# Performance work log

Hardware: AMD Instinct MI355X
Metric: run time of the kernel (lower is better)

The kernel has to match this reference:

```python
import jax, jax.numpy as jnp
import numpy as np

N_NODES = 50000
N_EDGES = 800000
DROP_P = 0.1


def setup_inputs() -> dict:
    key = jax.random.key(0)
    ks = jax.random.split(key, 8)
    x = jax.random.normal(ks[0], (N_NODES, 128), dtype=jnp.float32)
    edge_index = jax.random.randint(ks[1], (2, N_EDGES), 0, N_NODES, dtype=jnp.int64)
    # SAGEConv params: lin_l (applied to aggregated neighbors, has bias), lin_r (root, no bias)
    Wl1 = jax.random.normal(ks[2], (128, 256), dtype=jnp.float32) * 0.05
    Wr1 = jax.random.normal(ks[3], (128, 256), dtype=jnp.float32) * 0.05
    b1 = jax.random.normal(ks[4], (256,), dtype=jnp.float32) * 0.05
    Wl2 = jax.random.normal(ks[5], (256, 128), dtype=jnp.float32) * 0.05
    Wr2 = jax.random.normal(ks[6], (256, 128), dtype=jnp.float32) * 0.05
    b2 = jax.random.normal(ks[7], (128,), dtype=jnp.float32) * 0.05
    return {"x": x, "edge_index": edge_index, "Wl1": Wl1, "Wr1": Wr1, "b1": b1,
            "Wl2": Wl2, "Wr2": Wr2, "b2": b2}


def _sage_conv(x, src, dst, Wl, Wr, b, n_nodes):
    # PyG SAGEConv (mean aggr): out = lin_l(mean_{j in N(i)} x_j) + lin_r(x_i)
    msg = x[src]                                                  # [E, d] gather
    agg = jax.ops.segment_sum(msg, dst, num_segments=n_nodes)    # [N, d]
    cnt = jax.ops.segment_sum(jnp.ones((src.shape[0],), x.dtype), dst, num_segments=n_nodes)
    mean = agg / jnp.maximum(cnt, 1.0)[:, None]
    return mean @ Wl + x @ Wr + b


def reference(x, edge_index, Wl1, Wr1, b1, Wl2, Wr2, b2):
    src, dst = edge_index[0], edge_index[1]
    n = x.shape[0]
    h = _sage_conv(x, src, dst, Wl1, Wr1, b1, n)
    h = jax.nn.relu(h)
    # dropout p=0.1 with deterministic key (training=True in source)
    keep = jax.random.bernoulli(jax.random.key(42), 1.0 - DROP_P, h.shape)
    h = jnp.where(keep, h / (1.0 - DROP_P), 0.0)
    return _sage_conv(h, src, dst, Wl2, Wr2, b2, n)
```

## Files before the change

kernel.cpp:

```cpp
#include <hip/hip_runtime.h>

#define NN 50000
#define NE 800000
#define NBC 49
#define MSB 782

typedef __attribute__((ext_vector_type(8))) short short8;
typedef __attribute__((ext_vector_type(4))) float f32x4;

#define GLDS(g, l)                                                              \
  __builtin_amdgcn_global_load_lds(                                             \
      (const __attribute__((address_space(1))) void*)(g),                       \
      (__attribute__((address_space(3))) void*)(l), 16, 0, 0)

__device__ __forceinline__ unsigned short f2bf(float f) {
  union { float f; unsigned u; } v; v.f = f;
  unsigned r = (v.u + 0x7FFFu + ((v.u >> 16) & 1u)) >> 16;
  return (unsigned short)r;
}
__device__ __forceinline__ float bflo(unsigned u) {
  union { unsigned x; float f; } v; v.x = u << 16; return v.f;
}
__device__ __forceinline__ float bfhi(unsigned u) {
  union { unsigned x; float f; } v; v.x = u & 0xFFFF0000u; return v.f;
}

__device__ __forceinline__ unsigned tf_rotl(unsigned x, int r) {
#if __has_builtin(__builtin_amdgcn_alignbit)
  return __builtin_amdgcn_alignbit(x, x, 32 - r);
#else
  return (x << r) | (x >> (32 - r));
#endif
}
__device__ __forceinline__ void threefry_0_42(unsigned x0, unsigned x1,
                                              unsigned& o0, unsigned& o1) {
  const unsigned k0 = 0u, k1 = 42u;
  const unsigned k2 = k0 ^ k1 ^ 0x1BD11BDAu;
  x0 += k0; x1 += k1;
#define TF_R(r) { x0 += x1; x1 = tf_rotl(x1, (r)); x1 ^= x0; }
  TF_R(13) TF_R(15) TF_R(26) TF_R(6)
  x0 += k1; x1 += k2 + 1u;
  TF_R(17) TF_R(29) TF_R(16) TF_R(24)
  x0 += k2; x1 += k0 + 2u;
  TF_R(13) TF_R(15) TF_R(26) TF_R(6)
  x0 += k0; x1 += k1 + 3u;
  TF_R(17) TF_R(29) TF_R(16) TF_R(24)
  x0 += k1; x1 += k2 + 4u;
  TF_R(13) TF_R(15) TF_R(26) TF_R(6)
  x0 += k2; x1 += k0 + 5u;
#undef TF_R
  o0 = x0; o1 = x1;
}

#define CVTB 6250
#define MSKW 400000
#define MSKB 1563
__global__ void prep_k(const float4* __restrict__ x, uint2* __restrict__ xb,
                       const float* __restrict__ Wl1, const float* __restrict__ Wr1,
                       const float* __restrict__ Wl2, const float* __restrict__ Wr2,
                       unsigned short* __restrict__ W1t, unsigned short* __restrict__ W2t,
                       unsigned* __restrict__ msk, unsigned* __restrict__ hist) {
  int bid = blockIdx.x;
  if (bid < CVTB) {
    int i = bid * 256 + threadIdx.x;
    float4 v = x[i];
    uint2 o;
    o.x = (unsigned)f2bf(v.x) | ((unsigned)f2bf(v.y) << 16);
    o.y = (unsigned)f2bf(v.z) | ((unsigned)f2bf(v.w) << 16);
    xb[i] = o;
  } else if (bid < CVTB + 512) {
    int gid = (bid - CVTB) * 256 + threadIdx.x;
    int idx = gid & 65535;
    int n = idx >> 8, k = idx & 255;
    if (gid < 65536) {
      float v = (k < 128) ? Wr1[(size_t)k * 256 + n] : Wl1[(size_t)(k - 128) * 256 + n];
      W1t[idx] = f2bf(v);
    } else {
      float v = (n < 128) ? Wl2[(size_t)k * 128 + n] : Wr2[(size_t)k * 128 + (n - 128)];
      W2t[idx] = f2bf(v);
    }
  } else if (bid < CVTB + 512 + MSKB) {
    int w = (bid - CVTB - 512) * 256 + threadIdx.x;
    if (w < MSKW) {
      unsigned base = (unsigned)w * 32u;
      unsigned m = 0;
#pragma unroll
      for (int b = 0; b < 32; ++b) {
        unsigned o0, o1;
        threefry_0_42(0u, base + (unsigned)b, o0, o1);
        if (((o0 ^ o1) >> 9) < 7549747u) m |= (1u << b);
      }
      msk[w] = m;
    }
  } else {
    if (threadIdx.x < 64) hist[threadIdx.x] = 0;
  }
}

__global__ __launch_bounds__(256) void histC_k(const int* __restrict__ dst,
                                               unsigned* __restrict__ hist) {
  __shared__ unsigned lh[64];
  int tid = threadIdx.x;
  if (tid < 64) lh[tid] = 0;
  __syncthreads();
  int base = blockIdx.x * 1024;
#pragma unroll
  for (int k = 0; k < 4; ++k) {
    int e = base + k * 256 + tid;
    if (e < NE) atomicAdd(&lh[((unsigned)dst[e]) >> 10], 1u);
  }
  __syncthreads();
  if (tid < 64 && lh[tid]) atomicAdd(&hist[tid], lh[tid]);
}

__global__ __launch_bounds__(64) void scan64_k(const unsigned* __restrict__ hist,
                                               unsigned* __restrict__ bases,
                                               unsigned* __restrict__ gcur) {
  int tid = threadIdx.x;
  unsigned v = hist[tid], incl = v;
#pragma unroll
  for (int o = 1; o < 64; o <<= 1) {
    unsigned t = __shfl_up(incl, o);
    if (tid >= o) incl += t;
  }
  unsigned ex = incl - v;
  bases[tid] = ex;
  gcur[tid] = ex;
  if (tid == 63) bases[64] = incl;
}

__global__ __launch_bounds__(256) void msplit_k(const int* __restrict__ src,
                                                const int* __restrict__ dst,
                                                unsigned* __restrict__ gcur,
                                                unsigned* __restrict__ bufA) {
  __shared__ unsigned lh[64], gb[64], lc[64];
  int tid = threadIdx.x;
  if (tid < 64) { lh[tid] = 0; lc[tid] = 0; }
  __syncthreads();
  int base = blockIdx.x * 1024;
  unsigned s[4], d[4];
  bool val[4];
#pragma unroll
  for (int k = 0; k < 4; ++k) {
    int e = base + k * 256 + tid;
    val[k] = (e < NE);
    s[k] = val[k] ? (unsigned)src[e] : 0u;
    d[k] = val[k] ? (unsigned)dst[e] : 0u;
    if (val[k]) atomicAdd(&lh[d[k] >> 10], 1u);
  }
  __syncthreads();
  if (tid < 64 && lh[tid]) gb[tid] = atomicAdd(&gcur[tid], lh[tid]);
  __syncthreads();
#pragma unroll
  for (int k = 0; k < 4; ++k) {
    if (val[k]) {
      unsigned b = d[k] >> 10;
      unsigned pos = atomicAdd(&lc[b], 1u);
      bufA[gb[b] + pos] = (s[k] & 0xFFFFu) | ((d[k] & 1023u) << 16);
    }
  }
}

__global__ __launch_bounds__(1024) void passB2_k(const unsigned* __restrict__ bases,
                                                 const unsigned* __restrict__ bufA,
                                                 unsigned short* __restrict__ esrc,
                                                 unsigned* __restrict__ rowptr,
                                                 float* __restrict__ inv) {
  __shared__ unsigned cnt[1024], offs[1024], s_[1024];
  __shared__ unsigned short stage[18432];
  const int b = blockIdx.x, tid = threadIdx.x;
  const unsigned base0 = bases[b];
  const unsigned end0 = bases[b + 1];
  const unsigned bcnt = end0 - base0;

  cnt[tid] = 0;
  __syncthreads();
  for (unsigned i = tid; i < bcnt; i += 1024)
    atomicAdd(&cnt[bufA[base0 + i] >> 16], 1u);
  __syncthreads();

  unsigned c = cnt[tid];
  s_[tid] = c;
  __syncthreads();
  for (int o = 1; o < 1024; o <<= 1) {
    unsigned t = (tid >= o) ? s_[tid - o] : 0u;
    __syncthreads();
    s_[tid] += t;
    __syncthreads();
  }
  unsigned ex = s_[tid] - c;
  offs[tid] = ex;
  int node = b * 1024 + tid;
  if (node < NN) {
    rowptr[node] = base0 + ex;
    inv[node] = 1.0f / fmaxf((float)c, 1.0f);
  }
  cnt[tid] = 0;
  if (b == NBC - 1 && tid == 0) rowptr[NN] = NE;
  __syncthreads();

  if (bcnt <= 18432) {
    for (unsigned i = tid; i < bcnt; i += 1024) {
      unsigned w = bufA[base0 + i];
      unsigned dl = w >> 16;
      unsigned pos = atomicAdd(&cnt[dl], 1u);
      stage[offs[dl] + pos] = (unsigned short)w;
    }
    __syncthreads();
    for (unsigned i = tid; i < bcnt; i += 1024) esrc[base0 + i] = stage[i];
  } else {
    for (unsigned i = tid; i < bcnt; i += 1024) {
      unsigned w = bufA[base0 + i];
      unsigned dl = w >> 16;
      unsigned pos = atomicAdd(&cnt[dl], 1u);
      esrc[base0 + offs[dl] + pos] = (unsigned short)w;
    }
  }
}

__global__ __launch_bounds__(256) void gather_mean_k(
    const unsigned short* __restrict__ esrc, const unsigned* __restrict__ rowptr,
    const float* __restrict__ inv, const unsigned* __restrict__ xb,
    unsigned* __restrict__ meanb) {
  int node = blockIdx.x * 4 + (threadIdx.x >> 6);
  if (node >= NN) return;
  int lane = threadIdx.x & 63;
  unsigned beg = rowptr[node], end = rowptr[node + 1];
  float ax = 0.f, ay = 0.f;
  unsigned t = beg;
  for (; t + 8 <= end; t += 8) {
    unsigned v0 = xb[(size_t)esrc[t + 0] * 64 + lane];
    unsigned v1 = xb[(size_t)esrc[t + 1] * 64 + lane];
    unsigned v2 = xb[(size_t)esrc[t + 2] * 64 + lane];
    unsigned v3 = xb[(size_t)esrc[t + 3] * 64 + lane];
    unsigned v4 = xb[(size_t)esrc[t + 4] * 64 + lane];
    unsigned v5 = xb[(size_t)esrc[t + 5] * 64 + lane];
    unsigned v6 = xb[(size_t)esrc[t + 6] * 64 + lane];
    unsigned v7 = xb[(size_t)esrc[t + 7] * 64 + lane];
    ax += ((bflo(v0) + bflo(v1)) + (bflo(v2) + bflo(v3))) +
          ((bflo(v4) + bflo(v5)) + (bflo(v6) + bflo(v7)));
    ay += ((bfhi(v0) + bfhi(v1)) + (bfhi(v2) + bfhi(v3))) +
          ((bfhi(v4) + bfhi(v5)) + (bfhi(v6) + bfhi(v7)));
  }
  for (; t + 4 <= end; t += 4) {
    unsigned v0 = xb[(size_t)esrc[t + 0] * 64 + lane];
    unsigned v1 = xb[(size_t)esrc[t + 1] * 64 + lane];
    unsigned v2 = xb[(size_t)esrc[t + 2] * 64 + lane];
    unsigned v3 = xb[(size_t)esrc[t + 3] * 64 + lane];
    ax += (bflo(v0) + bflo(v1)) + (bflo(v2) + bflo(v3));
    ay += (bfhi(v0) + bfhi(v1)) + (bfhi(v2) + bfhi(v3));
  }
  for (; t < end; ++t) {
    unsigned v0 = xb[(size_t)esrc[t] * 64 + lane];
    ax += bflo(v0); ay += bfhi(v0);
  }
  float sc = inv[node];
  meanb[(size_t)node * 64 + lane] =
      (unsigned)f2bf(ax * sc) | ((unsigned)f2bf(ay * sc) << 16);
}

__global__ __launch_bounds__(256) void gather_add_k(
    const unsigned short* __restrict__ esrc, const unsigned* __restrict__ rowptr,
    const float* __restrict__ inv, const unsigned* __restrict__ P,
    float* __restrict__ out) {
  int node = blockIdx.x * 4 + (threadIdx.x >> 6);
  if (node >= NN) return;
  int lane = threadIdx.x & 63;
  unsigned beg = rowptr[node], end = rowptr[node + 1];
  float ax = 0.f, ay = 0.f;
  unsigned t = beg;
  for (; t + 8 <= end; t += 8) {
    unsigned v0 = P[(size_t)esrc[t + 0] * 64 + lane];
    unsigned v1 = P[(size_t)esrc[t + 1] * 64 + lane];
    unsigned v2 = P[(size_t)esrc[t + 2] * 64 + lane];
    unsigned v3 = P[(size_t)esrc[t + 3] * 64 + lane];
    unsigned v4 = P[(size_t)esrc[t + 4] * 64 + lane];
    unsigned v5 = P[(size_t)esrc[t + 5] * 64 + lane];
    unsigned v6 = P[(size_t)esrc[t + 6] * 64 + lane];
    unsigned v7 = P[(size_t)esrc[t + 7] * 64 + lane];
    ax += ((bflo(v0) + bflo(v1)) + (bflo(v2) + bflo(v3))) +
          ((bflo(v4) + bflo(v5)) + (bflo(v6) + bflo(v7)));
    ay += ((bfhi(v0) + bfhi(v1)) + (bfhi(v2) + bfhi(v3))) +
          ((bfhi(v4) + bfhi(v5)) + (bfhi(v6) + bfhi(v7)));
  }
  for (; t + 4 <= end; t += 4) {
    unsigned v0 = P[(size_t)esrc[t + 0] * 64 + lane];
    unsigned v1 = P[(size_t)esrc[t + 1] * 64 + lane];
    unsigned v2 = P[(size_t)esrc[t + 2] * 64 + lane];
    unsigned v3 = P[(size_t)esrc[t + 3] * 64 + lane];
    ax += (bflo(v0) + bflo(v1)) + (bflo(v2) + bflo(v3));
    ay += (bfhi(v0) + bfhi(v1)) + (bfhi(v2) + bfhi(v3));
  }
  for (; t < end; ++t) {
    unsigned v0 = P[(size_t)esrc[t] * 64 + lane];
    ax += bflo(v0); ay += bfhi(v0);
  }
  float sc = inv[node];
  float2* O = (float2*)out;
  float2 o = O[(size_t)node * 64 + lane];
  o.x += ax * sc;
  o.y += ay * sc;
  O[(size_t)node * 64 + lane] = o;
}


__global__ __launch_bounds__(256) void mgemm1_k(
    const unsigned short* __restrict__ xb, const unsigned short* __restrict__ meanb,
    const unsigned short* __restrict__ W1t, const float* __restrict__ b1,
    const unsigned* __restrict__ msk, unsigned short* __restrict__ h) {
  __shared__ __align__(16) char As[64 * 64 * 2];
  __shared__ __align__(16) char Bs[64 * 64 * 2];
  const int tid = threadIdx.x;
  const int lane = tid & 63, wid = tid >> 6;
  const int wm = (wid >> 1) * 32, wn = (wid & 1) * 32;
  const int r16 = lane & 15, g = lane >> 4;
  const unsigned bid = blockIdx.x;
  const unsigned v_ = (bid & 7u) * 391u + (bid >> 3);
  const int m0 = (int)(v_ >> 2) * 64;
  const int j0 = (int)(v_ & 3u) * 64;
  const int wbase = (tid & ~63);

  const unsigned short* aSrcX[2];
  const unsigned short* aSrcM[2];
  const unsigned short* bSrc[2];
  char* ldsA[2];
  char* ldsB[2];
#pragma unroll
  for (int p = 0; p < 2; ++p) {
    int id = p * 256 + tid;
    int r = id >> 3, cb = id & 7;
    int grow = m0 + r;
    if (grow >= NN) grow = NN - 1;
    int swz = (cb ^ (r & 7)) << 3;
    aSrcX[p] = xb + (size_t)grow * 128 + swz;
    aSrcM[p] = meanb + (size_t)grow * 128 + swz;
    bSrc[p] = W1t + (size_t)(j0 + r) * 256 + swz;
    ldsA[p] = As + ((p * 256 + wbase) << 4);
    ldsB[p] = Bs + ((p * 256 + wbase) << 4);
  }

  int aoff[2][2], boff[2][2];
#pragma unroll
  for (int f = 0; f < 2; ++f)
#pragma unroll
    for (int ks = 0; ks < 2; ++ks) {
      int ar = wm + f * 16 + r16;
      aoff[f][ks] = ar * 128 + ((ks * 64 + g * 16) ^ ((ar & 7) << 4));
      int br = wn + f * 16 + r16;
      boff[f][ks] = br * 128 + ((ks * 64 + g * 16) ^ ((br & 7) << 4));
    }

  f32x4 acc[2][2] = {};

  auto compute = [&]() {
#pragma unroll
    for (int ks = 0; ks < 2; ++ks) {
      short8 af[2], bf[2];
#pragma unroll
      for (int f = 0; f < 2; ++f) {
        af[f] = *(const short8*)(As + aoff[f][ks]);
        bf[f] = *(const short8*)(Bs + boff[f][ks]);
      }
#pragma unroll
      for (int i = 0; i < 2; ++i)
#pragma unroll
        for (int j = 0; j < 2; ++j)
          acc[i][j] = __builtin_amdgcn_mfma_f32_16x16x32_bf16(af[i], bf[j], acc[i][j], 0, 0, 0);
    }
  };

  GLDS(aSrcX[0], ldsA[0]); GLDS(aSrcX[1], ldsA[1]);
  GLDS(bSrc[0], ldsB[0]);  GLDS(bSrc[1], ldsB[1]);
  __syncthreads();
  compute();
  __syncthreads();
  GLDS(aSrcX[0] + 64, ldsA[0]); GLDS(aSrcX[1] + 64, ldsA[1]);
  GLDS(bSrc[0] + 64, ldsB[0]);  GLDS(bSrc[1] + 64, ldsB[1]);
  __syncthreads();
  compute();
  __syncthreads();
  GLDS(aSrcM[0], ldsA[0]);       GLDS(aSrcM[1], ldsA[1]);
  GLDS(bSrc[0] + 128, ldsB[0]);  GLDS(bSrc[1] + 128, ldsB[1]);
  __syncthreads();
  compute();
  __syncthreads();
  GLDS(aSrcM[0] + 64, ldsA[0]);  GLDS(aSrcM[1] + 64, ldsA[1]);
  GLDS(bSrc[0] + 192, ldsB[0]);  GLDS(bSrc[1] + 192, ldsB[1]);
  __syncthreads();
  compute();

#pragma unroll
  for (int i = 0; i < 2; ++i)
#pragma unroll
    for (int j = 0; j < 2; ++j) {
      int col = j0 + wn + j * 16 + r16;
      float bias = b1[col];
#pragma unroll
      for (int q = 0; q < 4; ++q) {
        int row = m0 + wm + i * 16 + g * 4 + q;
        if (row < NN) {
          unsigned flat = (unsigned)row * 256u + (unsigned)col;
          unsigned keep = (msk[flat >> 5] >> (flat & 31u)) & 1u;
          float v = fmaxf(acc[i][j][q] + bias, 0.f) * (keep ? (1.0f / 0.9f) : 0.f);
          h[(size_t)row * 256 + col] = f2bf(v);
        }
      }
    }
}

__global__ __launch_bounds__(256) void mgemm2_k(
    const unsigned short* __restrict__ h, const unsigned short* __restrict__ W2t,
    const float* __restrict__ b2, unsigned short* __restrict__ P,
    float* __restrict__ out) {
  __shared__ __align__(16) char As[64 * 64 * 2];
  __shared__ __align__(16) char Bs[64 * 64 * 2];
  const int tid = threadIdx.x;
  const int lane = tid & 63, wid = tid >> 6;
  const int wm = (wid >> 1) * 32, wn = (wid & 1) * 32;
  const int r16 = lane & 15, g = lane >> 4;
  const unsigned bid = blockIdx.x;
  const unsigned v_ = (bid & 7u) * 391u + (bid >> 3);
  const int m0 = (int)(v_ >> 2) * 64;
  const int j0 = (int)(v_ & 3u) * 64;
  const int wbase = (tid & ~63);

  const unsigned short* aSrc[2];
  const unsigned short* bSrc[2];
  char* ldsA[2];
  char* ldsB[2];
#pragma unroll
  for (int p = 0; p < 2; ++p) {
    int id = p * 256 + tid;
    int r = id >> 3, cb = id & 7;
    int grow = m0 + r;
    if (grow >= NN) grow = NN - 1;
    int swz = (cb ^ (r & 7)) << 3;
    aSrc[p] = h + (size_t)grow * 256 + swz;
    bSrc[p] = W2t + (size_t)(j0 + r) * 256 + swz;
    ldsA[p] = As + ((p * 256 + wbase) << 4);
    ldsB[p] = Bs + ((p * 256 + wbase) << 4);
  }

  int aoff[2][2], boff[2][2];
#pragma unroll
  for (int f = 0; f < 2; ++f)
#pragma unroll
    for (int ks = 0; ks < 2; ++ks) {
      int ar = wm + f * 16 + r16;
      aoff[f][ks] = ar * 128 + ((ks * 64 + g * 16) ^ ((ar & 7) << 4));
      int br = wn + f * 16 + r16;
      boff[f][ks] = br * 128 + ((ks * 64 + g * 16) ^ ((br & 7) << 4));
    }

  f32x4 acc[2][2] = {};

  auto compute = [&]() {
#pragma unroll
    for (int ks = 0; ks < 2; ++ks) {
      short8 af[2], bf[2];
#pragma unroll
      for (int f = 0; f < 2; ++f) {
        af[f] = *(const short8*)(As + aoff[f][ks]);
        bf[f] = *(const short8*)(Bs + boff[f][ks]);
      }
#pragma unroll
      for (int i = 0; i < 2; ++i)
#pragma unroll
        for (int j = 0; j < 2; ++j)
          acc[i][j] = __builtin_amdgcn_mfma_f32_16x16x32_bf16(af[i], bf[j], acc[i][j], 0, 0, 0);
    }
  };

  GLDS(aSrc[0], ldsA[0]); GLDS(aSrc[1], ldsA[1]);
  GLDS(bSrc[0], ldsB[0]); GLDS(bSrc[1], ldsB[1]);
  __syncthreads();
  compute();
  __syncthreads();
  GLDS(aSrc[0] + 64, ldsA[0]); GLDS(aSrc[1] + 64, ldsA[1]);
  GLDS(bSrc[0] + 64, ldsB[0]); GLDS(bSrc[1] + 64, ldsB[1]);
  __syncthreads();
  compute();
  __syncthreads();
  GLDS(aSrc[0] + 128, ldsA[0]); GLDS(aSrc[1] + 128, ldsA[1]);
  GLDS(bSrc[0] + 128, ldsB[0]); GLDS(bSrc[1] + 128, ldsB[1]);
  __syncthreads();
  compute();
  __syncthreads();
  GLDS(aSrc[0] + 192, ldsA[0]); GLDS(aSrc[1] + 192, ldsA[1]);
  GLDS(bSrc[0] + 192, ldsB[0]); GLDS(bSrc[1] + 192, ldsB[1]);
  __syncthreads();
  compute();

#pragma unroll
  for (int i = 0; i < 2; ++i)
#pragma unroll
    for (int j = 0; j < 2; ++j) {
      int col = j0 + wn + j * 16 + r16;
#pragma unroll
      for (int q = 0; q < 4; ++q) {
        int row = m0 + wm + i * 16 + g * 4 + q;
        if (row < NN) {
          if (col < 128) {
            P[(size_t)row * 128 + col] = f2bf(acc[i][j][q]);
          } else {
            out[(size_t)row * 128 + (col - 128)] = acc[i][j][q] + b2[col - 128];
          }
        }
      }
    }
}

extern "C" void kernel_launch(void* const* d_in, const int* in_sizes, int n_in,
                              void* d_out, int out_size, void* d_ws, size_t ws_size,
                              hipStream_t stream) {
  const float* x   = (const float*)d_in[0];
  const int*   ei  = (const int*)d_in[1];
  const float* Wl1 = (const float*)d_in[2];
  const float* Wr1 = (const float*)d_in[3];
  const float* b1  = (const float*)d_in[4];
  const float* Wl2 = (const float*)d_in[5];
  const float* Wr2 = (const float*)d_in[6];
  const float* b2  = (const float*)d_in[7];
  float* out = (float*)d_out;

  const int* src = ei;
  const int* dst = ei + NE;

  char* ws = (char*)d_ws;
  unsigned*       rowptr = (unsigned*)ws;
  float*          inv    = (float*)(ws + 0x40000);
  unsigned*       hist   = (unsigned*)(ws + 0x80000);
  unsigned*       bases  = (unsigned*)(ws + 0x80400);
  unsigned*       gcur   = (unsigned*)(ws + 0x80800);
  unsigned short* esrc   = (unsigned short*)(ws + 0xC0000);
  unsigned*       bufA   = (unsigned*)(ws + 0x280000);
  unsigned short* W1t    = (unsigned short*)(ws + 0x600000);
  unsigned short* W2t    = (unsigned short*)(ws + 0x620000);
  unsigned short* xb     = (unsigned short*)(ws + 0x700000);
  unsigned short* meanb  = (unsigned short*)(ws + 0x1400000);
  unsigned short* h      = (unsigned short*)(ws + 0x2100000);
  unsigned short* P      = (unsigned short*)(ws + 0x3A00000);
  unsigned*       msk    = (unsigned*)(ws + 0x3A00000);

  const int TPB = 256;

  prep_k<<<CVTB + 512 + MSKB + 1, TPB, 0, stream>>>(
      (const float4*)x, (uint2*)xb, Wl1, Wr1, Wl2, Wr2, W1t, W2t, msk, hist);

  histC_k<<<MSB, TPB, 0, stream>>>(dst, hist);
  scan64_k<<<1, 64, 0, stream>>>(hist, bases, gcur);
  msplit_k<<<MSB, TPB, 0, stream>>>(src, dst, gcur, bufA);
  passB2_k<<<NBC, 1024, 0, stream>>>(bases, bufA, esrc, rowptr, inv);

  gather_mean_k<<<(NN + 3) / 4, TPB, 0, stream>>>(esrc, rowptr, inv, (const unsigned*)xb, (unsigned*)meanb);
  mgemm1_k<<<3128, TPB, 0, stream>>>(xb, meanb, W1t, b1, msk, h);

  mgemm2_k<<<3128, TPB, 0, stream>>>(h, W2t, b2, P, out);
  gather_add_k<<<(NN + 3) / 4, TPB, 0, stream>>>(esrc, rowptr, inv, (const unsigned*)P, out);
}
```

Before: 196.6 us.

## Fuse dropout RNG into first GEMM epilogue and halve edge-split block count

Drops the separate dropout-mask generation pass from the prep kernel and instead computes the threefry-based keep/scale per output element inside mgemm1, issued right after the first async tile loads so it can overlap with them. This removes the mask buffer write and read and a large part of the prep launch. In exchange each GEMM thread runs 16 threefry evaluations, which adds ALU work and register pressure to the GEMM. The histogram and split kernels also now process 2048 edges per block instead of 1024, halving their grid size.

```diff
diff --git a/kernel.cpp b/kernel.cpp
--- a/kernel.cpp
+++ b/kernel.cpp
@@ -3,7 +3,7 @@
 #define NN 50000
 #define NE 800000
 #define NBC 49
-#define MSB 782
+#define MSB 391
 
 typedef __attribute__((ext_vector_type(8))) short short8;
 typedef __attribute__((ext_vector_type(4))) float f32x4;
@@ -51,15 +51,19 @@
 #undef TF_R
   o0 = x0; o1 = x1;
 }
+__device__ __forceinline__ float dropout_scale(unsigned flat) {
+  unsigned o0, o1;
+  threefry_0_42(0u, flat, o0, o1);
+  unsigned bits = o0 ^ o1;
+  return ((bits >> 9) < 7549747u) ? (1.0f / 0.9f) : 0.0f;
+}
 
 #define CVTB 6250
-#define MSKW 400000
-#define MSKB 1563
 __global__ void prep_k(const float4* __restrict__ x, uint2* __restrict__ xb,
                        const float* __restrict__ Wl1, const float* __restrict__ Wr1,
                        const float* __restrict__ Wl2, const float* __restrict__ Wr2,
                        unsigned short* __restrict__ W1t, unsigned short* __restrict__ W2t,
-                       unsigned* __restrict__ msk, unsigned* __restrict__ hist) {
+                       unsigned* __restrict__ hist) {
   int bid = blockIdx.x;
   if (bid < CVTB) {
     int i = bid * 256 + threadIdx.x;
@@ -79,19 +83,6 @@
       float v = (n < 128) ? Wl2[(size_t)k * 128 + n] : Wr2[(size_t)k * 128 + (n - 128)];
       W2t[idx] = f2bf(v);
     }
-  } else if (bid < CVTB + 512 + MSKB) {
-    int w = (bid - CVTB - 512) * 256 + threadIdx.x;
-    if (w < MSKW) {
-      unsigned base = (unsigned)w * 32u;
-      unsigned m = 0;
-#pragma unroll
-      for (int b = 0; b < 32; ++b) {
-        unsigned o0, o1;
-        threefry_0_42(0u, base + (unsigned)b, o0, o1);
-        if (((o0 ^ o1) >> 9) < 7549747u) m |= (1u << b);
-      }
-      msk[w] = m;
-    }
   } else {
     if (threadIdx.x < 64) hist[threadIdx.x] = 0;
   }
@@ -103,9 +94,9 @@
   int tid = threadIdx.x;
   if (tid < 64) lh[tid] = 0;
   __syncthreads();
-  int base = blockIdx.x * 1024;
-#pragma unroll
-  for (int k = 0; k < 4; ++k) {
+  int base = blockIdx.x * 2048;
+#pragma unroll
+  for (int k = 0; k < 8; ++k) {
     int e = base + k * 256 + tid;
     if (e < NE) atomicAdd(&lh[((unsigned)dst[e]) >> 10], 1u);
   }
@@ -137,11 +128,11 @@
   int tid = threadIdx.x;
   if (tid < 64) { lh[tid] = 0; lc[tid] = 0; }
   __syncthreads();
-  int base = blockIdx.x * 1024;
-  unsigned s[4], d[4];
-  bool val[4];
-#pragma unroll
-  for (int k = 0; k < 4; ++k) {
+  int base = blockIdx.x * 2048;
+  unsigned s[8], d[8];
+  bool val[8];
+#pragma unroll
+  for (int k = 0; k < 8; ++k) {
     int e = base + k * 256 + tid;
     val[k] = (e < NE);
     s[k] = val[k] ? (unsigned)src[e] : 0u;
@@ -152,7 +143,7 @@
   if (tid < 64 && lh[tid]) gb[tid] = atomicAdd(&gcur[tid], lh[tid]);
   __syncthreads();
 #pragma unroll
-  for (int k = 0; k < 4; ++k) {
+  for (int k = 0; k < 8; ++k) {
     if (val[k]) {
       unsigned b = d[k] >> 10;
       unsigned pos = atomicAdd(&lc[b], 1u);
@@ -307,7 +298,7 @@
 __global__ __launch_bounds__(256) void mgemm1_k(
     const unsigned short* __restrict__ xb, const unsigned short* __restrict__ meanb,
     const unsigned short* __restrict__ W1t, const float* __restrict__ b1,
-    const unsigned* __restrict__ msk, unsigned short* __restrict__ h) {
+    unsigned short* __restrict__ h) {
   __shared__ __align__(16) char As[64 * 64 * 2];
   __shared__ __align__(16) char Bs[64 * 64 * 2];
   const int tid = threadIdx.x;
@@ -371,6 +362,20 @@
 
   GLDS(aSrcX[0], ldsA[0]); GLDS(aSrcX[1], ldsA[1]);
   GLDS(bSrc[0], ldsB[0]);  GLDS(bSrc[1], ldsB[1]);
+
+  float dsc[2][2][4];
+#pragma unroll
+  for (int i = 0; i < 2; ++i)
+#pragma unroll
+    for (int j = 0; j < 2; ++j) {
+      int col = j0 + wn + j * 16 + r16;
+#pragma unroll
+      for (int q = 0; q < 4; ++q) {
+        int row = m0 + wm + i * 16 + g * 4 + q;
+        dsc[i][j][q] = dropout_scale((unsigned)row * 256u + (unsigned)col);
+      }
+    }
+
   __syncthreads();
   compute();
   __syncthreads();
@@ -399,9 +404,7 @@
       for (int q = 0; q < 4; ++q) {
         int row = m0 + wm + i * 16 + g * 4 + q;
         if (row < NN) {
-          unsigned flat = (unsigned)row * 256u + (unsigned)col;
-          unsigned keep = (msk[flat >> 5] >> (flat & 31u)) & 1u;
-          float v = fmaxf(acc[i][j][q] + bias, 0.f) * (keep ? (1.0f / 0.9f) : 0.f);
+          float v = fmaxf(acc[i][j][q] + bias, 0.f) * dsc[i][j][q];
           h[(size_t)row * 256 + col] = f2bf(v);
         }
       }
@@ -540,12 +543,11 @@
   unsigned short* meanb  = (unsigned short*)(ws + 0x1400000);
   unsigned short* h      = (unsigned short*)(ws + 0x2100000);
   unsigned short* P      = (unsigned short*)(ws + 0x3A00000);
-  unsigned*       msk    = (unsigned*)(ws + 0x3A00000);
 
   const int TPB = 256;
 
-  prep_k<<<CVTB + 512 + MSKB + 1, TPB, 0, stream>>>(
-      (const float4*)x, (uint2*)xb, Wl1, Wr1, Wl2, Wr2, W1t, W2t, msk, hist);
+  prep_k<<<CVTB + 513, TPB, 0, stream>>>((const float4*)x, (uint2*)xb,
+                                         Wl1, Wr1, Wl2, Wr2, W1t, W2t, hist);
 
   histC_k<<<MSB, TPB, 0, stream>>>(dst, hist);
   scan64_k<<<1, 64, 0, stream>>>(hist, bases, gcur);
@@ -553,7 +555,7 @@
   passB2_k<<<NBC, 1024, 0, stream>>>(bases, bufA, esrc, rowptr, inv);
 
   gather_mean_k<<<(NN + 3) / 4, TPB, 0, stream>>>(esrc, rowptr, inv, (const unsigned*)xb, (unsigned*)meanb);
-  mgemm1_k<<<3128, TPB, 0, stream>>>(xb, meanb, W1t, b1, msk, h);
+  mgemm1_k<<<3128, TPB, 0, stream>>>(xb, meanb, W1t, b1, h);
 
   mgemm2_k<<<3128, TPB, 0, stream>>>(h, W2t, b2, P, out);
   gather_add_k<<<(NN + 3) / 4, TPB, 0, stream>>>(esrc, rowptr, inv, (const unsigned*)P, out);
```

Result: faster. 171.1 us (-13.0%).
